# Kernel tuning notes

Measured on AMD Instinct MI355X. Metric: run time of the kernel, lower is better.

The kernel has to match this reference:

```python
import jax, jax.numpy as jnp
import numpy as np

NUM_USERS = 50000
NUM_ITEMS = 50000
N_NODES = NUM_USERS + NUM_ITEMS
NNZ = 3200000
EMB_DIM = 64
N_LAYERS = 3
BATCH = 16384


def setup_inputs() -> dict:
    key = jax.random.key(0)
    ks = jax.random.split(key, 7)
    user_emb = 0.1 * jax.random.normal(ks[0], (NUM_USERS, EMB_DIM), dtype=jnp.float32)
    item_emb = 0.1 * jax.random.normal(ks[1], (NUM_ITEMS, EMB_DIM), dtype=jnp.float32)
    edge_val = jax.random.uniform(ks[2], (NNZ,), dtype=jnp.float32)
    edge_src = jax.random.randint(ks[3], (NNZ,), 0, N_NODES, dtype=jnp.int32)
    edge_dst = jax.random.randint(ks[4], (NNZ,), 0, N_NODES, dtype=jnp.int32)
    users = jax.random.randint(ks[5], (BATCH,), 0, NUM_USERS, dtype=jnp.int32)
    items = jax.random.randint(ks[6], (BATCH,), 0, NUM_ITEMS, dtype=jnp.int32)
    return {"user_emb": user_emb, "item_emb": item_emb, "edge_val": edge_val,
            "edge_src": edge_src, "edge_dst": edge_dst, "users": users, "items": items}


def _computer(user_emb, item_emb, edge_val, edge_src, edge_dst):
    # LightGCN propagation: all_emb <- A @ all_emb, mean over layer outputs (incl. layer 0)
    all_emb = jnp.concatenate([user_emb, item_emb], axis=0)  # [N, D]
    acc = all_emb
    for _ in range(N_LAYERS):
        msg = edge_val[:, None] * all_emb[edge_src]          # [nnz, D]
        all_emb = jax.ops.segment_sum(msg, edge_dst, num_segments=N_NODES)
        acc = acc + all_emb
    light_out = acc / jnp.float32(N_LAYERS + 1)
    return light_out[:NUM_USERS], light_out[NUM_USERS:]


def reference(user_emb, item_emb, edge_val, edge_src, edge_dst, users, items):
    all_users, all_items = _computer(user_emb, item_emb, edge_val, edge_src, edge_dst)
    users_emb = all_users[users]                              # [B, D]
    items_emb = all_items[items]                              # [B, D]
    gamma = jnp.sum(users_emb * items_emb, axis=1)            # [B]
    return gamma
```

## Files before the change

kernel.cpp:

```cpp
#include <hip/hip_runtime.h>

#define NUM_USERS 50000
#define NUM_ITEMS 50000
#define N_NODES   100000
#define NNZ       3200000
#define EMB_DIM   64
#define N_LAYERS  3
#define BATCH     16384

#define NBUCK 512
#define ABITS 8
#define NODES_PER_BUCK 256
#define TILE_EDGES 8192
#define NBUCK_USED ((N_NODES + NODES_PER_BUCK - 1) / NODES_PER_BUCK)
#define CAP 9216

typedef unsigned long long ull;

__device__ inline unsigned bf16pair(float a, float b) {
    unsigned ua = __float_as_uint(a), ub = __float_as_uint(b);
    unsigned r0 = (ua + 0x7fffu + ((ua >> 16) & 1u)) >> 16;
    unsigned r1 = (ub + 0x7fffu + ((ub >> 16) & 1u)) >> 16;
    return r0 | (r1 << 16);
}
__device__ inline float blo(unsigned u) { return __uint_as_float(u << 16); }
__device__ inline float bhi(unsigned u) { return __uint_as_float(u & 0xffff0000u); }

__device__ inline void acc8(float* s, uint4 g, float w) {
    s[0] = fmaf(w, blo(g.x), s[0]); s[1] = fmaf(w, bhi(g.x), s[1]);
    s[2] = fmaf(w, blo(g.y), s[2]); s[3] = fmaf(w, bhi(g.y), s[3]);
    s[4] = fmaf(w, blo(g.z), s[4]); s[5] = fmaf(w, bhi(g.z), s[5]);
    s[6] = fmaf(w, blo(g.w), s[6]); s[7] = fmaf(w, bhi(g.w), s[7]);
}

__global__ void init_emb_kernel(const float* __restrict__ ue,
                                const float* __restrict__ ie,
                                unsigned* __restrict__ E0,
                                int* __restrict__ bucketCursor,
                                unsigned char* __restrict__ flags,
                                const int* __restrict__ users,
                                const int* __restrict__ items) {
    int idx = blockIdx.x * blockDim.x + threadIdx.x;
    if (blockIdx.x == 0 && threadIdx.x < 256) {
        bucketCursor[threadIdx.x]       = threadIdx.x * CAP;
        bucketCursor[threadIdx.x + 256] = (threadIdx.x + 256) * CAP;
    }
    if (idx < BATCH) {
        flags[users[idx]] = 1;
    } else if (idx < 2 * BATCH) {
        flags[NUM_USERS + items[idx - BATCH]] = 1;
    }
    const int total = N_NODES * (EMB_DIM / 4);
    if (idx >= total) return;
    const int uoff = NUM_USERS * (EMB_DIM / 4);
    float4 v;
    if (idx < uoff) v = ((const float4*)ue)[idx];
    else            v = ((const float4*)ie)[idx - uoff];
    uint2 h;
    h.x = bf16pair(v.x, v.y);
    h.y = bf16pair(v.z, v.w);
    ((uint2*)E0)[idx] = h;
}

__global__ void partA_kernel(const float* __restrict__ ev,
                             const int*  __restrict__ es,
                             const int*  __restrict__ ed,
                             int* __restrict__ bucketCursor,
                             ull* __restrict__ tmp) {
    __shared__ int hist[NBUCK];
    __shared__ int base[NBUCK];
    __shared__ int cnt2[NBUCK];
    int tid = threadIdx.x;
    int e0 = blockIdx.x * TILE_EDGES;

    int      mySrc[8], myDst[8];
    unsigned myQ[8];

    for (int i = tid; i < NBUCK; i += 1024) hist[i] = 0;
    __syncthreads();

    #pragma unroll
    for (int k = 0; k < 8; ++k) {
        int e = e0 + k * 1024 + tid;
        if (e < NNZ) {
            mySrc[k] = es[e];
            myDst[k] = ed[e];
            myQ[k]   = (unsigned)fminf(ev[e] * 32768.f + 0.5f, 32767.f);
            atomicAdd(&hist[((unsigned)myDst[k]) >> ABITS], 1);
        } else {
            myDst[k] = -1;
        }
    }
    __syncthreads();

    for (int i = tid; i < NBUCK; i += 1024) {
        int c = hist[i];
        base[i] = c ? atomicAdd(&bucketCursor[i], c) : 0;
        cnt2[i] = 0;
    }
    __syncthreads();

    #pragma unroll
    for (int k = 0; k < 8; ++k) {
        int dst = myDst[k];
        if (dst < 0) continue;
        int b = ((unsigned)dst) >> ABITS;
        int pos = base[b] + atomicAdd(&cnt2[b], 1);
        if (pos < (b + 1) * CAP) {
            ull rec = (ull)(unsigned)(mySrc[k] | ((dst & (NODES_PER_BUCK - 1)) << 17))
                    | ((ull)myQ[k] << 25);
            tmp[pos] = rec;
        }
    }
}

__global__ void partB_kernel(const ull* __restrict__ tmp,
                             const int* __restrict__ bucketCursor,
                             int* __restrict__ rowStart,
                             int* __restrict__ deg,
                             unsigned* __restrict__ sorted) {
    __shared__ int cnt[NODES_PER_BUCK];
    __shared__ int sc[NODES_PER_BUCK];
    __shared__ int cur[NODES_PER_BUCK];
    int b = blockIdx.x;
    int tid = threadIdx.x;
    int nodeLo = b << ABITS;
    int startE = b * CAP;
    int endE   = bucketCursor[b];

    if (tid < NODES_PER_BUCK) cnt[tid] = 0;
    __syncthreads();

    ull myRec[9];
    int nRec = 0;
    #pragma unroll
    for (int k = 0; k < 9; ++k) {
        int i = startE + k * 1024 + tid;
        if (i < endE) {
            myRec[k] = tmp[i];
            nRec = k + 1;
            atomicAdd(&cnt[(int)((myRec[k] >> 17) & (NODES_PER_BUCK - 1))], 1);
        }
    }
    __syncthreads();

    if (tid < NODES_PER_BUCK) sc[tid] = cnt[tid];
    __syncthreads();
    for (int o = 1; o < NODES_PER_BUCK; o <<= 1) {
        int add = 0;
        if (tid < NODES_PER_BUCK && tid >= o) add = sc[tid - o];
        __syncthreads();
        if (tid < NODES_PER_BUCK) sc[tid] += add;
        __syncthreads();
    }
    if (tid < NODES_PER_BUCK) {
        int node = nodeLo + tid;
        int rs = startE + sc[tid] - cnt[tid];
        cur[tid] = rs;
        if (node < N_NODES) {
            rowStart[node] = rs;
            deg[node] = cnt[tid];
        }
    }
    __syncthreads();

    for (int k = 0; k < nRec; ++k) {
        ull rec = myRec[k];
        int dl = (int)((rec >> 17) & (NODES_PER_BUCK - 1));
        unsigned o = (unsigned)(rec & 0x1FFFFULL) | ((unsigned)((rec >> 25) & 0x7FFF) << 17);
        int pos = atomicAdd(&cur[dl], 1);
        sorted[pos] = o;
    }
}

__global__ void pull_kernel(const uint4* __restrict__ A16,
                            uint4* __restrict__ B16,
                            const unsigned* __restrict__ sorted,
                            const int* __restrict__ rowStart,
                            const int* __restrict__ deg,
                            const unsigned char* __restrict__ flags,
                            int gate) {
    int t = blockIdx.x * blockDim.x + threadIdx.x;
    int node = t >> 6;
    if (node >= N_NODES) return;
    if (gate && flags[node] != 1) return;
    int lane = t & 63;
    int eg = lane >> 3;
    int d8 = lane & 7;
    int start = rowStart[node];
    int cnt   = deg[node];
    const unsigned* ep = sorted + start;
    const float k15 = 1.f / 32768.f;

    float s[8] = {0.f,0.f,0.f,0.f,0.f,0.f,0.f,0.f};
    int j = 0;
    while (j + 32 <= cnt) {
        unsigned r0 = ep[j + eg], r1 = ep[j + 8 + eg];
        unsigned r2 = ep[j + 16 + eg], r3 = ep[j + 24 + eg];
        uint4 g0 = A16[(((long long)(r0 & 0x1FFFFu)) << 3) + d8];
        uint4 g1 = A16[(((long long)(r1 & 0x1FFFFu)) << 3) + d8];
        uint4 g2 = A16[(((long long)(r2 & 0x1FFFFu)) << 3) + d8];
        uint4 g3 = A16[(((long long)(r3 & 0x1FFFFu)) << 3) + d8];
        acc8(s, g0, (float)(r0 >> 17) * k15);
        acc8(s, g1, (float)(r1 >> 17) * k15);
        acc8(s, g2, (float)(r2 >> 17) * k15);
        acc8(s, g3, (float)(r3 >> 17) * k15);
        j += 32;
    }
    while (j + 16 <= cnt) {
        unsigned r0 = ep[j + eg], r1 = ep[j + 8 + eg];
        uint4 g0 = A16[(((long long)(r0 & 0x1FFFFu)) << 3) + d8];
        uint4 g1 = A16[(((long long)(r1 & 0x1FFFFu)) << 3) + d8];
        acc8(s, g0, (float)(r0 >> 17) * k15);
        acc8(s, g1, (float)(r1 >> 17) * k15);
        j += 16;
    }
    for (; j < cnt; j += 8) {
        int idx = j + eg;
        unsigned r = (idx < cnt) ? ep[idx] : 0u;
        uint4 g = A16[(((long long)(r & 0x1FFFFu)) << 3) + d8];
        acc8(s, g, (float)(r >> 17) * k15);
    }
    #pragma unroll
    for (int k = 0; k < 8; ++k) {
        s[k] += __shfl_xor(s[k], 8, 64);
        s[k] += __shfl_xor(s[k], 16, 64);
        s[k] += __shfl_xor(s[k], 32, 64);
    }
    if (eg == 0) {
        uint4 h;
        h.x = bf16pair(s[0], s[1]);
        h.y = bf16pair(s[2], s[3]);
        h.z = bf16pair(s[4], s[5]);
        h.w = bf16pair(s[6], s[7]);
        B16[(((long long)node) << 3) + d8] = h;
    }
}

__global__ void dot_kernel(const unsigned* __restrict__ E0,
                           const unsigned* __restrict__ B1,
                           const unsigned* __restrict__ B2,
                           const unsigned* __restrict__ B3,
                           const int* __restrict__ users,
                           const int* __restrict__ items,
                           float* __restrict__ out) {
    int t = blockIdx.x * blockDim.x + threadIdx.x;
    int b = t >> 5;
    int lane = t & 31;
    if (b >= BATCH) return;
    long long uo = ((long long)users[b] << 5) + lane;
    long long io = ((long long)(items[b] + NUM_USERS) << 5) + lane;
    unsigned a0 = E0[uo], a1 = B1[uo], a2 = B2[uo], a3 = B3[uo];
    unsigned c0 = E0[io], c1 = B1[io], c2 = B2[io], c3 = B3[io];
    float ux = (blo(a0) + blo(a1)) + (blo(a2) + blo(a3));
    float uy = (bhi(a0) + bhi(a1)) + (bhi(a2) + bhi(a3));
    float ix = (blo(c0) + blo(c1)) + (blo(c2) + blo(c3));
    float iy = (bhi(c0) + bhi(c1)) + (bhi(c2) + bhi(c3));
    float p = ux * ix + uy * iy;
    #pragma unroll
    for (int off = 16; off >= 1; off >>= 1)
        p += __shfl_xor(p, off, 64);
    if (lane == 0) out[b] = p * 0.0625f;
}

extern "C" void kernel_launch(void* const* d_in, const int* in_sizes, int n_in,
                              void* d_out, int out_size, void* d_ws, size_t ws_size,
                              hipStream_t stream) {
    const float* user_emb = (const float*)d_in[0];
    const float* item_emb = (const float*)d_in[1];
    const float* edge_val = (const float*)d_in[2];
    const int*   edge_src = (const int*)d_in[3];
    const int*   edge_dst = (const int*)d_in[4];
    const int*   users    = (const int*)d_in[5];
    const int*   items    = (const int*)d_in[6];
    float* out = (float*)d_out;

    const size_t emb16Bytes = (size_t)N_NODES * EMB_DIM * 2;
    const size_t sortBytes  = (size_t)NBUCK_USED * CAP * sizeof(unsigned);
    const size_t tmpBytes   = (size_t)NBUCK_USED * CAP * sizeof(ull);
    const size_t nodeBytes  = (size_t)N_NODES * sizeof(int);

    char* w = (char*)d_ws;
    unsigned* E0           = (unsigned*)(w); w += emb16Bytes;
    unsigned* B1           = (unsigned*)(w); w += emb16Bytes;
    unsigned* B2           = (unsigned*)(w); w += emb16Bytes;
    unsigned* B3           = (unsigned*)(w); w += emb16Bytes;
    unsigned* sorted       = (unsigned*)(w); w += sortBytes;
    ull*      tmp          = (ull*)(w);      w += tmpBytes;
    int*      deg          = (int*)(w);      w += nodeBytes;
    int*      rowStart     = (int*)(w);      w += nodeBytes;
    int*      bucketCursor = (int*)(w);      w += NBUCK * sizeof(int);
    unsigned char* flags   = (unsigned char*)(w); w += N_NODES;

    const int vecTotal   = N_NODES * (EMB_DIM / 4);
    const int initBlocks = (vecTotal + 255) / 256;
    const int tileBlocks = (NNZ + TILE_EDGES - 1) / TILE_EDGES;

    init_emb_kernel<<<initBlocks, 256, 0, stream>>>(user_emb, item_emb, E0,
                                                    bucketCursor, flags, users, items);

    partA_kernel<<<tileBlocks, 1024, 0, stream>>>(edge_val, edge_src, edge_dst,
                                                  bucketCursor, tmp);
    partB_kernel<<<NBUCK_USED, 1024, 0, stream>>>(tmp, bucketCursor,
                                                  rowStart, deg, sorted);

    const int pullBlocks = (N_NODES * 64 + 255) / 256;
    pull_kernel<<<pullBlocks, 256, 0, stream>>>((const uint4*)E0, (uint4*)B1,
                                                sorted, rowStart, deg, flags, 0);
    pull_kernel<<<pullBlocks, 256, 0, stream>>>((const uint4*)B1, (uint4*)B2,
                                                sorted, rowStart, deg, flags, 0);
    pull_kernel<<<pullBlocks, 256, 0, stream>>>((const uint4*)B2, (uint4*)B3,
                                                sorted, rowStart, deg, flags, 1);

    const int dotBlocks = (BATCH * 32 + 255) / 256;
    dot_kernel<<<dotBlocks, 256, 0, stream>>>(E0, B1, B2, B3, users, items, out);
}
```

Before: 281.8 us.

## Pad CSR rows to multiples of four and vectorize pull gather with packed FMA

```diff
diff --git a/kernel.cpp b/kernel.cpp
--- a/kernel.cpp
+++ b/kernel.cpp
@@ -16,6 +16,7 @@
 #define CAP 9216
 
 typedef unsigned long long ull;
+typedef float v2f __attribute__((ext_vector_type(2)));
 
 __device__ inline unsigned bf16pair(float a, float b) {
     unsigned ua = __float_as_uint(a), ub = __float_as_uint(b);
@@ -26,11 +27,26 @@
 __device__ inline float blo(unsigned u) { return __uint_as_float(u << 16); }
 __device__ inline float bhi(unsigned u) { return __uint_as_float(u & 0xffff0000u); }
 
-__device__ inline void acc8(float* s, uint4 g, float w) {
-    s[0] = fmaf(w, blo(g.x), s[0]); s[1] = fmaf(w, bhi(g.x), s[1]);
-    s[2] = fmaf(w, blo(g.y), s[2]); s[3] = fmaf(w, bhi(g.y), s[3]);
-    s[4] = fmaf(w, blo(g.z), s[4]); s[5] = fmaf(w, bhi(g.z), s[5]);
-    s[6] = fmaf(w, blo(g.w), s[6]); s[7] = fmaf(w, bhi(g.w), s[7]);
+__device__ inline void pkfma(v2f& d, v2f a, v2f b) {
+    asm("v_pk_fma_f32 %0, %1, %2, %0" : "+v"(d) : "v"(a), "v"(b));
+}
+
+__device__ inline void accP(v2f& sA, v2f& sB, v2f& sC, v2f& sD, uint4 g, unsigned r) {
+    float w = (float)(r >> 17);
+    v2f w2 = {w, w};
+    v2f e0 = {blo(g.x), bhi(g.x)};
+    v2f e1 = {blo(g.y), bhi(g.y)};
+    v2f e2 = {blo(g.z), bhi(g.z)};
+    v2f e3 = {blo(g.w), bhi(g.w)};
+    pkfma(sA, e0, w2);
+    pkfma(sB, e1, w2);
+    pkfma(sC, e2, w2);
+    pkfma(sD, e3, w2);
+}
+
+__device__ inline uint4 gath(const unsigned char* __restrict__ base, unsigned r, unsigned dOff) {
+    unsigned off = ((r & 0x1FFFFu) << 7) + dOff;
+    return *(const uint4*)(base + off);
 }
 
 __global__ void init_emb_kernel(const float* __restrict__ ue,
@@ -144,7 +160,7 @@
     }
     __syncthreads();
 
-    if (tid < NODES_PER_BUCK) sc[tid] = cnt[tid];
+    if (tid < NODES_PER_BUCK) sc[tid] = (cnt[tid] + 3) & ~3;
     __syncthreads();
     for (int o = 1; o < NODES_PER_BUCK; o <<= 1) {
         int add = 0;
@@ -155,7 +171,8 @@
     }
     if (tid < NODES_PER_BUCK) {
         int node = nodeLo + tid;
-        int rs = startE + sc[tid] - cnt[tid];
+        int pc = (cnt[tid] + 3) & ~3;
+        int rs = startE + sc[tid] - pc;
         cur[tid] = rs;
         if (node < N_NODES) {
             rowStart[node] = rs;
@@ -169,71 +186,81 @@
         int dl = (int)((rec >> 17) & (NODES_PER_BUCK - 1));
         unsigned o = (unsigned)(rec & 0x1FFFFULL) | ((unsigned)((rec >> 25) & 0x7FFF) << 17);
         int pos = atomicAdd(&cur[dl], 1);
-        sorted[pos] = o;
-    }
-}
-
-__global__ void pull_kernel(const uint4* __restrict__ A16,
+        if (pos < startE + CAP) sorted[pos] = o;
+    }
+}
+
+__global__ void pull_kernel(const unsigned char* __restrict__ A16,
                             uint4* __restrict__ B16,
                             const unsigned* __restrict__ sorted,
                             const int* __restrict__ rowStart,
                             const int* __restrict__ deg,
                             const unsigned char* __restrict__ flags,
                             int gate) {
-    int t = blockIdx.x * blockDim.x + threadIdx.x;
-    int node = t >> 6;
+    int node = __builtin_amdgcn_readfirstlane((blockIdx.x << 2) + (threadIdx.x >> 6));
     if (node >= N_NODES) return;
     if (gate && flags[node] != 1) return;
-    int lane = t & 63;
+    int lane = threadIdx.x & 63;
     int eg = lane >> 3;
-    int d8 = lane & 7;
+    unsigned dOff = (unsigned)(lane & 7) << 4;
     int start = rowStart[node];
     int cnt   = deg[node];
     const unsigned* ep = sorted + start;
-    const float k15 = 1.f / 32768.f;
-
-    float s[8] = {0.f,0.f,0.f,0.f,0.f,0.f,0.f,0.f};
+
+    v2f sA = {0.f, 0.f}, sB = {0.f, 0.f}, sC = {0.f, 0.f}, sD = {0.f, 0.f};
     int j = 0;
     while (j + 32 <= cnt) {
-        unsigned r0 = ep[j + eg], r1 = ep[j + 8 + eg];
-        unsigned r2 = ep[j + 16 + eg], r3 = ep[j + 24 + eg];
-        uint4 g0 = A16[(((long long)(r0 & 0x1FFFFu)) << 3) + d8];
-        uint4 g1 = A16[(((long long)(r1 & 0x1FFFFu)) << 3) + d8];
-        uint4 g2 = A16[(((long long)(r2 & 0x1FFFFu)) << 3) + d8];
-        uint4 g3 = A16[(((long long)(r3 & 0x1FFFFu)) << 3) + d8];
-        acc8(s, g0, (float)(r0 >> 17) * k15);
-        acc8(s, g1, (float)(r1 >> 17) * k15);
-        acc8(s, g2, (float)(r2 >> 17) * k15);
-        acc8(s, g3, (float)(r3 >> 17) * k15);
+        uint4 R = *(const uint4*)(ep + j + (eg << 2));
+        uint4 g0 = gath(A16, R.x, dOff);
+        uint4 g1 = gath(A16, R.y, dOff);
+        uint4 g2 = gath(A16, R.z, dOff);
+        uint4 g3 = gath(A16, R.w, dOff);
+        accP(sA, sB, sC, sD, g0, R.x);
+        accP(sA, sB, sC, sD, g1, R.y);
+        accP(sA, sB, sC, sD, g2, R.z);
+        accP(sA, sB, sC, sD, g3, R.w);
         j += 32;
     }
-    while (j + 16 <= cnt) {
-        unsigned r0 = ep[j + eg], r1 = ep[j + 8 + eg];
-        uint4 g0 = A16[(((long long)(r0 & 0x1FFFFu)) << 3) + d8];
-        uint4 g1 = A16[(((long long)(r1 & 0x1FFFFu)) << 3) + d8];
-        acc8(s, g0, (float)(r0 >> 17) * k15);
-        acc8(s, g1, (float)(r1 >> 17) * k15);
-        j += 16;
-    }
-    for (; j < cnt; j += 8) {
-        int idx = j + eg;
-        unsigned r = (idx < cnt) ? ep[idx] : 0u;
-        uint4 g = A16[(((long long)(r & 0x1FFFFu)) << 3) + d8];
-        acc8(s, g, (float)(r >> 17) * k15);
-    }
-    #pragma unroll
-    for (int k = 0; k < 8; ++k) {
-        s[k] += __shfl_xor(s[k], 8, 64);
-        s[k] += __shfl_xor(s[k], 16, 64);
-        s[k] += __shfl_xor(s[k], 32, 64);
-    }
+    int rem = cnt - j;
+    if (rem >= 16) {
+        uint2 R = *(const uint2*)(ep + j + (eg << 1));
+        uint4 g0 = gath(A16, R.x, dOff);
+        uint4 g1 = gath(A16, R.y, dOff);
+        accP(sA, sB, sC, sD, g0, R.x);
+        accP(sA, sB, sC, sD, g1, R.y);
+        j += 16; rem -= 16;
+    }
+    if (rem > 0) {
+        int i0 = j + eg, i1 = j + 8 + eg;
+        unsigned r0 = (i0 < cnt) ? ep[i0] : 0u;
+        unsigned r1 = (i1 < cnt) ? ep[i1] : 0u;
+        uint4 g0 = gath(A16, r0, dOff);
+        uint4 g1 = gath(A16, r1, dOff);
+        accP(sA, sB, sC, sD, g0, r0);
+        accP(sA, sB, sC, sD, g1, r1);
+    }
+
+    sA.x += __shfl_xor(sA.x, 8, 64);  sA.y += __shfl_xor(sA.y, 8, 64);
+    sB.x += __shfl_xor(sB.x, 8, 64);  sB.y += __shfl_xor(sB.y, 8, 64);
+    sC.x += __shfl_xor(sC.x, 8, 64);  sC.y += __shfl_xor(sC.y, 8, 64);
+    sD.x += __shfl_xor(sD.x, 8, 64);  sD.y += __shfl_xor(sD.y, 8, 64);
+    sA.x += __shfl_xor(sA.x, 16, 64); sA.y += __shfl_xor(sA.y, 16, 64);
+    sB.x += __shfl_xor(sB.x, 16, 64); sB.y += __shfl_xor(sB.y, 16, 64);
+    sC.x += __shfl_xor(sC.x, 16, 64); sC.y += __shfl_xor(sC.y, 16, 64);
+    sD.x += __shfl_xor(sD.x, 16, 64); sD.y += __shfl_xor(sD.y, 16, 64);
+    sA.x += __shfl_xor(sA.x, 32, 64); sA.y += __shfl_xor(sA.y, 32, 64);
+    sB.x += __shfl_xor(sB.x, 32, 64); sB.y += __shfl_xor(sB.y, 32, 64);
+    sC.x += __shfl_xor(sC.x, 32, 64); sC.y += __shfl_xor(sC.y, 32, 64);
+    sD.x += __shfl_xor(sD.x, 32, 64); sD.y += __shfl_xor(sD.y, 32, 64);
+
     if (eg == 0) {
+        const float k15 = 1.f / 32768.f;
         uint4 h;
-        h.x = bf16pair(s[0], s[1]);
-        h.y = bf16pair(s[2], s[3]);
-        h.z = bf16pair(s[4], s[5]);
-        h.w = bf16pair(s[6], s[7]);
-        B16[(((long long)node) << 3) + d8] = h;
+        h.x = bf16pair(sA.x * k15, sA.y * k15);
+        h.y = bf16pair(sB.x * k15, sB.y * k15);
+        h.z = bf16pair(sC.x * k15, sC.y * k15);
+        h.w = bf16pair(sD.x * k15, sD.y * k15);
+        B16[(((long long)node) << 3) + (lane & 7)] = h;
     }
 }
 
@@ -305,11 +332,11 @@
                                                   rowStart, deg, sorted);
 
     const int pullBlocks = (N_NODES * 64 + 255) / 256;
-    pull_kernel<<<pullBlocks, 256, 0, stream>>>((const uint4*)E0, (uint4*)B1,
+    pull_kernel<<<pullBlocks, 256, 0, stream>>>((const unsigned char*)E0, (uint4*)B1,
                                                 sorted, rowStart, deg, flags, 0);
-    pull_kernel<<<pullBlocks, 256, 0, stream>>>((const uint4*)B1, (uint4*)B2,
+    pull_kernel<<<pullBlocks, 256, 0, stream>>>((const unsigned char*)B1, (uint4*)B2,
                                                 sorted, rowStart, deg, flags, 0);
-    pull_kernel<<<pullBlocks, 256, 0, stream>>>((const uint4*)B2, (uint4*)B3,
+    pull_kernel<<<pullBlocks, 256, 0, stream>>>((const unsigned char*)B2, (uint4*)B3,
                                                 sorted, rowStart, deg, flags, 1);
 
     const int dotBlocks = (BATCH * 32 + 255) / 256;
```

New measurement: 277.7 us. Within noise of the previous version (-1.4%).
